# Kernel tuning notes

Hardware: AMD Instinct MI355X
Metric: run time of the kernel (lower is better)

## Reference

```python
import jax, jax.numpy as jnp
import numpy as np

H = 1024      # hidden_size
NH = 16       # num_heads
DH = H // NH  # size_per_head
RV = 32       # relative_vocab_size
B, S = 1, 2048


def setup_inputs() -> dict:
    key = jax.random.key(0)
    ks = jax.random.split(key, 12)
    std = 0.02
    inp = {
        'x': jax.random.normal(ks[0], (B, S, H), jnp.float32),
        'att_mask': jnp.ones((B, S, S), jnp.int32),
        'relative_att_ids': jax.random.randint(ks[1], (B, S, S), 0, RV),
        'Wq': jax.random.normal(ks[2], (H, H), jnp.float32) * std,
        'bq': jnp.zeros((H,), jnp.float32),
        'Wk': jax.random.normal(ks[3], (H, H), jnp.float32) * std,
        'bk': jnp.zeros((H,), jnp.float32),
        'Wv': jax.random.normal(ks[4], (H, H), jnp.float32) * std,
        'bv': jnp.zeros((H,), jnp.float32),
        'rel_emb': jax.random.normal(ks[5], (RV, NH, DH), jnp.float32) * 0.5,
        'rel_bias': jnp.zeros((RV, NH), jnp.float32),
        'Wo': jax.random.normal(ks[6], (H, H), jnp.float32) * std,
        'bo': jnp.zeros((H,), jnp.float32),
    }
    return inp


def reference(x, att_mask, relative_att_ids, Wq, bq, Wk, bk, Wv, bv,
              rel_emb, rel_bias, Wo, bo):
    b, s, _ = x.shape
    # multi-head projections: [b, s, nh, dh]
    q = (x @ Wq + bq).reshape(b, s, NH, DH)
    k = (x @ Wk + bk).reshape(b, s, NH, DH)
    v = (x @ Wv + bv).reshape(b, s, NH, DH)

    # content scores: [b, q, k, h]
    content = jnp.einsum('bqhd,bkhd->bqkh', q, k)

    # relative scores over vocab: [b, q, r, h], then gather per key position
    all_rel = jnp.einsum('bqhd,rhd->bqrh', q, rel_emb) + rel_bias
    rel_scores = jnp.take_along_axis(all_rel, relative_att_ids[..., None], axis=2)

    scores = (content + rel_scores) / jnp.sqrt(jnp.asarray(DH, x.dtype))
    scores = scores + (-10000.0) * (1.0 - att_mask[..., None].astype(scores.dtype))

    probs = jax.nn.softmax(scores, axis=2)  # softmax over key dim (axis=-2)
    ctx = jnp.einsum('bqkh,bkhd->bqhd', probs, v).reshape(b, s, H)
    return ctx @ Wo + bo
```

## Files before the change

### kernel.cpp

```cpp
#include <hip/hip_runtime.h>
#include <hip/hip_bf16.h>

#define S 2048
#define H 1024
#define NH 16
#define DH 64
#define RV 32
#define BK 32
#define NSPLIT 2
#define SKEYS (S / NSPLIT)

typedef __hip_bfloat16 bf16;
typedef short bf16x8 __attribute__((ext_vector_type(8)));
typedef float f32x4 __attribute__((ext_vector_type(4)));

__device__ __forceinline__ float b2f(bf16 v) { return __bfloat162float(v); }
__device__ __forceinline__ unsigned short f2bbits(float x) {
    __hip_bfloat16 b = __float2bfloat16(x);
    return *reinterpret_cast<unsigned short*>(&b);
}
__device__ __forceinline__ float ldf(const void* p, int i, int f) {
    return f ? ((const float*)p)[i] : b2f(((const bf16*)p)[i]);
}
__device__ __forceinline__ void gl_lds16(const bf16* g, bf16* l) {
    __builtin_amdgcn_global_load_lds(
        (const __attribute__((address_space(1))) void*)g,
        (__attribute__((address_space(3))) void*)l,
        16, 0, 0);
}

__global__ void detect_dtype(const unsigned int* __restrict__ xw,
                             int* __restrict__ flag)
{
    __shared__ int cnt;
    if (threadIdx.x == 0) cnt = 0;
    __syncthreads();
    unsigned int w = xw[threadIdx.x];
    unsigned int ex = ((w & 0xffffu) >> 7) & 0xffu;
    int big = (ex > 134u) ? 1 : 0;
    #pragma unroll
    for (int off = 32; off > 0; off >>= 1) big += __shfl_xor(big, off, 64);
    if ((threadIdx.x & 63) == 0) atomicAdd(&cnt, big);
    __syncthreads();
    if (threadIdx.x == 0) *flag = (cnt > 60) ? 1 : 0;
}

__global__ __launch_bounds__(256) void pack_rm(
    const int* __restrict__ rel_ids, const int* __restrict__ att_mask,
    unsigned char* __restrict__ PBg)
{
    int i = blockIdx.x * 256 + threadIdx.x;
    int4 rid = ((const int4*)rel_ids)[i];
    int4 msk = ((const int4*)att_mask)[i];
    uchar4 o;
    o.x = (unsigned char)(rid.x | ((msk.x == 0) << 7));
    o.y = (unsigned char)(rid.y | ((msk.y == 0) << 7));
    o.z = (unsigned char)(rid.z | ((msk.z == 0) << 7));
    o.w = (unsigned char)(rid.w | ((msk.w == 0) << 7));
    ((uchar4*)PBg)[i] = o;
}

__global__ __launch_bounds__(256) void convert_x(
    const void* __restrict__ x, bf16* __restrict__ xb,
    const int* __restrict__ flag)
{
    const int i = (blockIdx.x * 256 + threadIdx.x) * 4;
    if (*flag) {
        float4 v = ((const float4*)x)[i >> 2];
        ushort4 o;
        o.x = f2bbits(v.x); o.y = f2bbits(v.y);
        o.z = f2bbits(v.z); o.w = f2bbits(v.w);
        *(ushort4*)&xb[i] = o;
    } else {
        ((ushort4*)xb)[i >> 2] = ((const ushort4*)x)[i >> 2];
    }
}

__global__ __launch_bounds__(256) void wtrans(
    const void* __restrict__ W0, const void* __restrict__ W1,
    const void* __restrict__ W2, const void* __restrict__ W3,
    bf16* __restrict__ T0, bf16* __restrict__ T1,
    bf16* __restrict__ T2, bf16* __restrict__ T3,
    const int* __restrict__ flag)
{
    const void* W; bf16* T;
    switch (blockIdx.z) {
        case 0:  W = W0; T = T0; break;
        case 1:  W = W1; T = T1; break;
        case 2:  W = W2; T = T2; break;
        default: W = W3; T = T3; break;
    }
    const int f = *flag;
    __shared__ unsigned short Ts[64][68];
    const int t = threadIdx.x;
    const int tx = t & 15, ty = t >> 4;
    const int n0 = blockIdx.x * 64;
    const int k0 = blockIdx.y * 64;
    #pragma unroll
    for (int it = 0; it < 4; ++it) {
        int k = ty + it * 16;
        int base = (k0 + k) * H + n0 + tx * 4;
        #pragma unroll
        for (int e = 0; e < 4; ++e)
            Ts[k][tx * 4 + e] = f2bbits(ldf(W, base + e, f));
    }
    __syncthreads();
    #pragma unroll
    for (int it = 0; it < 4; ++it) {
        int n = ty + it * 16;
        ushort4 o;
        o.x = Ts[tx * 4 + 0][n];
        o.y = Ts[tx * 4 + 1][n];
        o.z = Ts[tx * 4 + 2][n];
        o.w = Ts[tx * 4 + 3][n];
        *(ushort4*)&T[(size_t)(n0 + n) * H + k0 + tx * 4] = o;
    }
}

__global__ __launch_bounds__(256) void vtrans(
    const bf16* __restrict__ Vb, bf16* __restrict__ VT)
{
    __shared__ unsigned short Ts[64][68];
    const int t = threadIdx.x;
    const int tx = t & 15, ty = t >> 4;
    const int s0 = blockIdx.x * 64;
    const int h0 = blockIdx.y * 64;
    #pragma unroll
    for (int it = 0; it < 4; ++it) {
        int s = ty + it * 16;
        *(ushort4*)&Ts[s][tx * 4] =
            *(const ushort4*)&Vb[(size_t)(s0 + s) * H + h0 + tx * 4];
    }
    __syncthreads();
    #pragma unroll
    for (int it = 0; it < 4; ++it) {
        int hh = ty + it * 16;
        ushort4 o;
        o.x = Ts[tx * 4 + 0][hh];
        o.y = Ts[tx * 4 + 1][hh];
        o.z = Ts[tx * 4 + 2][hh];
        o.w = Ts[tx * 4 + 3][hh];
        *(ushort4*)&VT[(size_t)(h0 + hh) * S + s0 + tx * 4] = o;
    }
}

template<int BM, int BN>
__device__ __forceinline__ void gemm_bt_core(
    const bf16* __restrict__ A, const bf16* __restrict__ BT,
    f32x4 (&acc)[BM / 32][BN / 32])
{
    constexpr int MT = BM / 32, NT = BN / 32;
    const int tid = threadIdx.x;
    const int w = tid >> 6, lane = tid & 63;
    const int l15 = lane & 15, quad = lane >> 4;
    const int wm = (w & 1) * (BM / 2), wn = (w >> 1) * (BN / 2);
    const int rowb = blockIdx.y * BM;
    const int colb = blockIdx.x * BN;

    __shared__ bf16 As[BM * BK];
    __shared__ bf16 Bs[BN * BK];

    for (int kb = 0; kb < H; kb += BK) {
        #pragma unroll
        for (int j = 0; j < BM / 64; ++j) {
            int i = j * 256 + w * 64 + lane;
            gl_lds16(&A[(size_t)(rowb + (i >> 2)) * H + kb + (i & 3) * 8],
                     &As[(size_t)(j * 256 + w * 64) * 8]);
        }
        #pragma unroll
        for (int j = 0; j < BN / 64; ++j) {
            int i = j * 256 + w * 64 + lane;
            gl_lds16(&BT[(size_t)(colb + (i >> 2)) * H + kb + (i & 3) * 8],
                     &Bs[(size_t)(j * 256 + w * 64) * 8]);
        }
        __syncthreads();

        bf16x8 af[MT], bfr[NT];
        #pragma unroll
        for (int mt = 0; mt < MT; ++mt)
            af[mt] = *(const bf16x8*)&As[(wm + mt * 16 + l15) * BK + quad * 8];
        #pragma unroll
        for (int nt = 0; nt < NT; ++nt)
            bfr[nt] = *(const bf16x8*)&Bs[(wn + nt * 16 + l15) * BK + quad * 8];
        #pragma unroll
        for (int mt = 0; mt < MT; ++mt)
            #pragma unroll
            for (int nt = 0; nt < NT; ++nt)
                acc[mt][nt] = __builtin_amdgcn_mfma_f32_16x16x32_bf16(
                    af[mt], bfr[nt], acc[mt][nt], 0, 0, 0);
        __syncthreads();
    }
}

__global__ __launch_bounds__(256) void qkv_mfma(
    const bf16* __restrict__ xb,
    const bf16* __restrict__ WTq, const bf16* __restrict__ WTk,
    const bf16* __restrict__ WTv,
    const void* __restrict__ bq, const void* __restrict__ bk,
    const void* __restrict__ bv,
    bf16* __restrict__ Qb, bf16* __restrict__ Kb, bf16* __restrict__ Vb,
    const int* __restrict__ flag)
{
    const bf16* BT; const void* bias; bf16* out; float scale;
    if (blockIdx.z == 0)      { BT = WTq; bias = bq; out = Qb; scale = 1.0f;   }
    else if (blockIdx.z == 1) { BT = WTk; bias = bk; out = Kb; scale = 0.125f; }
    else                      { BT = WTv; bias = bv; out = Vb; scale = 1.0f;   }
    const int f = *flag;

    f32x4 acc[4][2];
    #pragma unroll
    for (int a = 0; a < 4; ++a)
        #pragma unroll
        for (int b = 0; b < 2; ++b) acc[a][b] = (f32x4)0.f;

    gemm_bt_core<128, 64>(xb, BT, acc);

    const int tid = threadIdx.x;
    const int w = tid >> 6, lane = tid & 63;
    const int l15 = lane & 15, quad = lane >> 4;
    const int wm = (w & 1) * 64, wn = (w >> 1) * 32;
    const int rowb = blockIdx.y * 128;
    const int colb = blockIdx.x * 64;

    float bvv[2];
    #pragma unroll
    for (int nt = 0; nt < 2; ++nt)
        bvv[nt] = ldf(bias, colb + wn + nt * 16 + l15, f);

    #pragma unroll
    for (int mt = 0; mt < 4; ++mt)
        #pragma unroll
        for (int nt = 0; nt < 2; ++nt)
            #pragma unroll
            for (int r = 0; r < 4; ++r) {
                int m = rowb + wm + mt * 16 + quad * 4 + r;
                int n = colb + wn + nt * 16 + l15;
                out[(size_t)m * H + n] =
                    __float2bfloat16((acc[mt][nt][r] + bvv[nt]) * scale);
            }
}

__global__ __launch_bounds__(256) void out_mfma(
    const bf16* __restrict__ Cb, const bf16* __restrict__ WoT,
    const void* __restrict__ bias, void* __restrict__ out,
    const int* __restrict__ flag)
{
    const int f = *flag;
    f32x4 acc[2][2];
    #pragma unroll
    for (int a = 0; a < 2; ++a)
        #pragma unroll
        for (int b = 0; b < 2; ++b) acc[a][b] = (f32x4)0.f;

    gemm_bt_core<64, 64>(Cb, WoT, acc);

    const int tid = threadIdx.x;
    const int w = tid >> 6, lane = tid & 63;
    const int l15 = lane & 15, quad = lane >> 4;
    const int wm = (w & 1) * 32, wn = (w >> 1) * 32;
    const int rowb = blockIdx.y * 64;
    const int colb = blockIdx.x * 64;

    float bvv[2];
    #pragma unroll
    for (int nt = 0; nt < 2; ++nt)
        bvv[nt] = ldf(bias, colb + wn + nt * 16 + l15, f);

    #pragma unroll
    for (int mt = 0; mt < 2; ++mt)
        #pragma unroll
        for (int nt = 0; nt < 2; ++nt)
            #pragma unroll
            for (int r = 0; r < 4; ++r) {
                int m = rowb + wm + mt * 16 + quad * 4 + r;
                int n = colb + wn + nt * 16 + l15;
                float v = acc[mt][nt][r] + bvv[nt];
                if (f) ((float*)out)[(size_t)m * H + n] = v;
                else   ((bf16*)out)[(size_t)m * H + n] = __float2bfloat16(v);
            }
}

__global__ __launch_bounds__(256, 4) void attn_mfma(
    const bf16* __restrict__ Qb, const bf16* __restrict__ Kb,
    const bf16* __restrict__ VT,
    const void* __restrict__ rel_emb, const void* __restrict__ rel_bias,
    const unsigned char* __restrict__ PBg,
    float* __restrict__ Op, float* __restrict__ Lp,
    const int* __restrict__ flag)
{
    const int h = blockIdx.x;
    const int qb = blockIdx.y;
    const int split = blockIdx.z;
    const int q0 = qb * 64;
    const int kt0 = split * SKEYS;
    const int tid = threadIdx.x;
    const int w = tid >> 6;
    const int lane = tid & 63;
    const int l15 = lane & 15;
    const int quad = lane >> 4;
    const int f = *flag;

    __shared__ short Ks[64][80];
    __shared__ short Vs[64][80];
    __shared__ float Rl[64][33];
    __shared__ float Rbias[32];
    union SharedU {
        short Es[32][64];
        short Ps[64][72];
    };
    __shared__ SharedU U;

    const unsigned char* pbrow = PBg + (size_t)(q0 + w * 16 + l15) * S;

    uint4 kp[2], vp[2];
    unsigned int pb[4];
    {
        #pragma unroll
        for (int j = 0; j < 2; ++j) {
            int slot = j * 256 + tid;
            int r = slot >> 3, c = slot & 7;
            kp[j] = *(const uint4*)&Kb[(size_t)(kt0 + r) * H + h * DH + c * 8];
            vp[j] = *(const uint4*)&VT[(size_t)(h * DH + r) * S + kt0 + c * 8];
        }
        #pragma unroll
        for (int nt = 0; nt < 4; ++nt)
            pb[nt] = *(const unsigned int*)&pbrow[kt0 + nt * 16 + quad * 4];
    }

    bf16x8 aq0, aq1;
    {
        const bf16* qrow = Qb + (size_t)(q0 + w * 16 + l15) * H + h * DH;
        aq0 = *(const bf16x8*)&qrow[quad * 8];
        aq1 = *(const bf16x8*)&qrow[32 + quad * 8];
    }

    {
        int r = tid >> 3, c8 = (tid & 7) * 8;
        unsigned short os[8];
        if (f) {
            const float* src = (const float*)rel_emb + (r * NH + h) * DH + c8;
            #pragma unroll
            for (int e = 0; e < 8; ++e) os[e] = f2bbits(src[e] * 0.125f);
        } else {
            const bf16* src = (const bf16*)rel_emb + (r * NH + h) * DH + c8;
            #pragma unroll
            for (int e = 0; e < 8; ++e) os[e] = f2bbits(b2f(src[e]) * 0.125f);
        }
        *(ushort4*)&U.Es[r][c8]     = *(ushort4*)&os[0];
        *(ushort4*)&U.Es[r][c8 + 4] = *(ushort4*)&os[4];
        if (tid < RV) Rbias[tid] = ldf(rel_bias, tid * NH + h, f) * 0.125f;
    }
    __syncthreads();

    #pragma unroll
    for (int nt = 0; nt < 2; ++nt) {
        bf16x8 be0 = *(const bf16x8*)&U.Es[nt * 16 + l15][quad * 8];
        bf16x8 be1 = *(const bf16x8*)&U.Es[nt * 16 + l15][32 + quad * 8];
        f32x4 c = (f32x4)0.f;
        c = __builtin_amdgcn_mfma_f32_16x16x32_bf16(aq0, be0, c, 0, 0, 0);
        c = __builtin_amdgcn_mfma_f32_16x16x32_bf16(aq1, be1, c, 0, 0, 0);
        float rb = Rbias[nt * 16 + l15];
        #pragma unroll
        for (int r = 0; r < 4; ++r)
            Rl[w * 16 + quad * 4 + r][nt * 16 + l15] = c[r] + rb;
    }
    __syncthreads();

    f32x4 O[4];
    #pragma unroll
    for (int i = 0; i < 4; ++i) O[i] = (f32x4)0.f;
    float llocal = 0.f;
    const float* rlrow = &Rl[w * 16 + l15][0];

    for (int kt = kt0; kt < kt0 + SKEYS; kt += 64) {
        #pragma unroll
        for (int j = 0; j < 2; ++j) {
            int slot = j * 256 + tid;
            int r = slot >> 3, c = slot & 7;
            *(uint4*)&Ks[r][c * 8] = kp[j];
            *(uint4*)&Vs[r][c * 8] = vp[j];
        }
        unsigned int pbc[4];
        #pragma unroll
        for (int nt = 0; nt < 4; ++nt) pbc[nt] = pb[nt];
        __syncthreads();

        if (kt + 64 < kt0 + SKEYS) {
            #pragma unroll
            for (int j = 0; j < 2; ++j) {
                int slot = j * 256 + tid;
                int r = slot >> 3, c = slot & 7;
                kp[j] = *(const uint4*)&Kb[(size_t)(kt + 64 + r) * H + h * DH + c * 8];
                vp[j] = *(const uint4*)&VT[(size_t)(h * DH + r) * S + kt + 64 + c * 8];
            }
            #pragma unroll
            for (int nt = 0; nt < 4; ++nt)
                pb[nt] = *(const unsigned int*)&pbrow[kt + 64 + nt * 16 + quad * 4];
        }

        f32x4 sc[4];
        #pragma unroll
        for (int nt = 0; nt < 4; ++nt) {
            bf16x8 ak0 = *(const bf16x8*)&Ks[nt * 16 + l15][quad * 8];
            bf16x8 ak1 = *(const bf16x8*)&Ks[nt * 16 + l15][32 + quad * 8];
            f32x4 c = (f32x4)0.f;
            c = __builtin_amdgcn_mfma_f32_16x16x32_bf16(ak0, aq0, c, 0, 0, 0);
            c = __builtin_amdgcn_mfma_f32_16x16x32_bf16(ak1, aq1, c, 0, 0, 0);
            sc[nt] = c;
        }

        #pragma unroll
        for (int nt = 0; nt < 4; ++nt) {
            unsigned int pw = pbc[nt];
            #pragma unroll
            for (int r = 0; r < 4; ++r) {
                unsigned int b = pw >> (8 * r);
                float rl = rlrow[b & 63u];
                float p = __expf(sc[nt][r] + rl);
                p = (b & 0x80u) ? 0.f : p;
                sc[nt][r] = p;
            }
            llocal += (sc[nt][0] + sc[nt][1]) + (sc[nt][2] + sc[nt][3]);
            ushort4 o;
            o.x = f2bbits(sc[nt][0]); o.y = f2bbits(sc[nt][1]);
            o.z = f2bbits(sc[nt][2]); o.w = f2bbits(sc[nt][3]);
            *(ushort4*)&U.Ps[w * 16 + l15][nt * 16 + quad * 4] = o;
        }

        bf16x8 ap0 = *(const bf16x8*)&U.Ps[w * 16 + l15][quad * 8];
        bf16x8 ap1 = *(const bf16x8*)&U.Ps[w * 16 + l15][32 + quad * 8];
        #pragma unroll
        for (int dt = 0; dt < 4; ++dt) {
            bf16x8 bv0 = *(const bf16x8*)&Vs[dt * 16 + l15][quad * 8];
            bf16x8 bv1 = *(const bf16x8*)&Vs[dt * 16 + l15][32 + quad * 8];
            O[dt] = __builtin_amdgcn_mfma_f32_16x16x32_bf16(ap0, bv0, O[dt], 0, 0, 0);
            O[dt] = __builtin_amdgcn_mfma_f32_16x16x32_bf16(ap1, bv1, O[dt], 0, 0, 0);
        }
        __syncthreads();
    }

    float lsum = llocal;
    lsum += __shfl_xor(lsum, 16, 64);
    lsum += __shfl_xor(lsum, 32, 64);

    const size_t base = ((size_t)split * NH + h) * 32 + qb;
    float* Ob = Op + base * 4096;
    #pragma unroll
    for (int r = 0; r < 4; ++r) {
        int qr = w * 16 + quad * 4 + r;
        #pragma unroll
        for (int dt = 0; dt < 4; ++dt)
            Ob[qr * 64 + dt * 16 + l15] = O[dt][r];
    }
    if (quad == 0) Lp[base * 64 + w * 16 + l15] = lsum;
}

__global__ __launch_bounds__(256) void reduce_splits(
    const float* __restrict__ Op, const float* __restrict__ Lp,
    bf16* __restrict__ Cb)
{
    const int h = blockIdx.x;
    const int qb = blockIdx.y;
    const int q0 = qb * 64;
    const int tid = threadIdx.x;
    const int q = tid >> 2;
    const int d0 = (tid & 3) * 16;

    const size_t b0 = ((size_t)0 * NH + h) * 32 + qb;
    const size_t b1 = ((size_t)1 * NH + h) * 32 + qb;

    float l = Lp[b0 * 64 + q] + Lp[b1 * 64 + q];
    float inv = 1.0f / l;

    const float4* O0 = (const float4*)(Op + b0 * 4096 + q * 64 + d0);
    const float4* O1 = (const float4*)(Op + b1 * 4096 + q * 64 + d0);
    bf16* outp = Cb + (size_t)(q0 + q) * H + h * DH + d0;
    #pragma unroll
    for (int j = 0; j < 4; ++j) {
        float4 v0 = O0[j], v1 = O1[j];
        ushort4 o;
        o.x = f2bbits((v0.x + v1.x) * inv);
        o.y = f2bbits((v0.y + v1.y) * inv);
        o.z = f2bbits((v0.z + v1.z) * inv);
        o.w = f2bbits((v0.w + v1.w) * inv);
        *(ushort4*)&outp[j * 4] = o;
    }
}

extern "C" void kernel_launch(void* const* d_in, const int* in_sizes, int n_in,
                              void* d_out, int out_size, void* d_ws, size_t ws_size,
                              hipStream_t stream)
{
    const void* x        = d_in[0];
    const int*  att_mask = (const int*)d_in[1];
    const int*  rel_ids  = (const int*)d_in[2];
    const void* Wq = d_in[3];
    const void* bq = d_in[4];
    const void* Wk = d_in[5];
    const void* bk = d_in[6];
    const void* Wv = d_in[7];
    const void* bv = d_in[8];
    const void* rel_emb  = d_in[9];
    const void* rel_bias = d_in[10];
    const void* Wo = d_in[11];
    const void* bo = d_in[12];

    char* p = (char*)d_ws;
    bf16* xb  = (bf16*)p; p += (size_t)S * H * 2;
    bf16* WTq = (bf16*)p; p += (size_t)H * H * 2;
    bf16* WTk = (bf16*)p; p += (size_t)H * H * 2;
    bf16* WTv = (bf16*)p; p += (size_t)H * H * 2;
    bf16* WoT = (bf16*)p; p += (size_t)H * H * 2;
    bf16* Qb  = (bf16*)p; p += (size_t)S * H * 2;
    bf16* Kb  = (bf16*)p; p += (size_t)S * H * 2;
    bf16* Vb  = (bf16*)p; p += (size_t)S * H * 2;
    bf16* VT  = (bf16*)p; p += (size_t)S * H * 2;
    bf16* Cb  = (bf16*)p; p += (size_t)S * H * 2;
    unsigned char* PBg = (unsigned char*)p; p += (size_t)S * S;
    float* Op = (float*)p; p += (size_t)NSPLIT * NH * 32 * 64 * 64 * 4;
    float* Lp = (float*)p; p += (size_t)NSPLIT * NH * 32 * 64 * 4;
    int* flag = (int*)p;

    detect_dtype<<<1, 256, 0, stream>>>((const unsigned int*)x, flag);

    pack_rm<<<(S * S) / 1024, 256, 0, stream>>>(rel_ids, att_mask, PBg);
    convert_x<<<(S * H) / 1024, 256, 0, stream>>>(x, xb, flag);
    wtrans<<<dim3(H / 64, H / 64, 4), 256, 0, stream>>>(
        Wq, Wk, Wv, Wo, WTq, WTk, WTv, WoT, flag);

    qkv_mfma<<<dim3(H / 64, S / 128, 3), 256, 0, stream>>>(
        xb, WTq, WTk, WTv, bq, bk, bv, Qb, Kb, Vb, flag);

    vtrans<<<dim3(S / 64, H / 64), 256, 0, stream>>>(Vb, VT);

    attn_mfma<<<dim3(NH, S / 64, NSPLIT), 256, 0, stream>>>(
        Qb, Kb, VT, rel_emb, rel_bias, PBg, Op, Lp, flag);

    reduce_splits<<<dim3(NH, S / 64), 256, 0, stream>>>(Op, Lp, Cb);

    out_mfma<<<dim3(H / 64, S / 64), 256, 0, stream>>>(Cb, WoT, bo, d_out, flag);
}
```

Baseline: 260.6 us.

## Load K/V fragments directly from global, drop LDS staging, split keys four ways

Removes the K and V shared-memory tiles and the register prefetch, so each wave loads its MFMA operands straight from global memory (relying on L1/L2 for reuse across the four waves). This eliminates two block barriers per key tile and frees LDS and registers. In exchange, the launch-bounds occupancy hint rises to 6 and the key dimension is split four ways instead of two, with the reduce kernel generalized to sum NSPLIT partials. The risks are redundant global traffic, since each wave rereads the same K/V, less latency hiding with no prefetch, and larger partial buffers for the reduction.

```diff
diff --git a/kernel.cpp b/kernel.cpp
--- a/kernel.cpp
+++ b/kernel.cpp
@@ -7,7 +7,7 @@
 #define DH 64
 #define RV 32
 #define BK 32
-#define NSPLIT 2
+#define NSPLIT 4
 #define SKEYS (S / NSPLIT)
 
 typedef __hip_bfloat16 bf16;
@@ -280,7 +280,7 @@
             }
 }
 
-__global__ __launch_bounds__(256, 4) void attn_mfma(
+__global__ __launch_bounds__(256, 6) void attn_mfma(
     const bf16* __restrict__ Qb, const bf16* __restrict__ Kb,
     const bf16* __restrict__ VT,
     const void* __restrict__ rel_emb, const void* __restrict__ rel_bias,
@@ -300,8 +300,6 @@
     const int quad = lane >> 4;
     const int f = *flag;
 
-    __shared__ short Ks[64][80];
-    __shared__ short Vs[64][80];
     __shared__ float Rl[64][33];
     __shared__ float Rbias[32];
     union SharedU {
@@ -309,23 +307,6 @@
         short Ps[64][72];
     };
     __shared__ SharedU U;
-
-    const unsigned char* pbrow = PBg + (size_t)(q0 + w * 16 + l15) * S;
-
-    uint4 kp[2], vp[2];
-    unsigned int pb[4];
-    {
-        #pragma unroll
-        for (int j = 0; j < 2; ++j) {
-            int slot = j * 256 + tid;
-            int r = slot >> 3, c = slot & 7;
-            kp[j] = *(const uint4*)&Kb[(size_t)(kt0 + r) * H + h * DH + c * 8];
-            vp[j] = *(const uint4*)&VT[(size_t)(h * DH + r) * S + kt0 + c * 8];
-        }
-        #pragma unroll
-        for (int nt = 0; nt < 4; ++nt)
-            pb[nt] = *(const unsigned int*)&pbrow[kt0 + nt * 16 + quad * 4];
-    }
 
     bf16x8 aq0, aq1;
     {
@@ -371,38 +352,20 @@
     for (int i = 0; i < 4; ++i) O[i] = (f32x4)0.f;
     float llocal = 0.f;
     const float* rlrow = &Rl[w * 16 + l15][0];
+    const unsigned char* pbrow = PBg + (size_t)(q0 + w * 16 + l15) * S;
 
     for (int kt = kt0; kt < kt0 + SKEYS; kt += 64) {
-        #pragma unroll
-        for (int j = 0; j < 2; ++j) {
-            int slot = j * 256 + tid;
-            int r = slot >> 3, c = slot & 7;
-            *(uint4*)&Ks[r][c * 8] = kp[j];
-            *(uint4*)&Vs[r][c * 8] = vp[j];
-        }
         unsigned int pbc[4];
         #pragma unroll
-        for (int nt = 0; nt < 4; ++nt) pbc[nt] = pb[nt];
-        __syncthreads();
-
-        if (kt + 64 < kt0 + SKEYS) {
-            #pragma unroll
-            for (int j = 0; j < 2; ++j) {
-                int slot = j * 256 + tid;
-                int r = slot >> 3, c = slot & 7;
-                kp[j] = *(const uint4*)&Kb[(size_t)(kt + 64 + r) * H + h * DH + c * 8];
-                vp[j] = *(const uint4*)&VT[(size_t)(h * DH + r) * S + kt + 64 + c * 8];
-            }
-            #pragma unroll
-            for (int nt = 0; nt < 4; ++nt)
-                pb[nt] = *(const unsigned int*)&pbrow[kt + 64 + nt * 16 + quad * 4];
-        }
+        for (int nt = 0; nt < 4; ++nt)
+            pbc[nt] = *(const unsigned int*)&pbrow[kt + nt * 16 + quad * 4];
 
         f32x4 sc[4];
         #pragma unroll
         for (int nt = 0; nt < 4; ++nt) {
-            bf16x8 ak0 = *(const bf16x8*)&Ks[nt * 16 + l15][quad * 8];
-            bf16x8 ak1 = *(const bf16x8*)&Ks[nt * 16 + l15][32 + quad * 8];
+            const bf16* krow = Kb + (size_t)(kt + nt * 16 + l15) * H + h * DH;
+            bf16x8 ak0 = *(const bf16x8*)&krow[quad * 8];
+            bf16x8 ak1 = *(const bf16x8*)&krow[32 + quad * 8];
             f32x4 c = (f32x4)0.f;
             c = __builtin_amdgcn_mfma_f32_16x16x32_bf16(ak0, aq0, c, 0, 0, 0);
             c = __builtin_amdgcn_mfma_f32_16x16x32_bf16(ak1, aq1, c, 0, 0, 0);
@@ -431,12 +394,12 @@
         bf16x8 ap1 = *(const bf16x8*)&U.Ps[w * 16 + l15][32 + quad * 8];
         #pragma unroll
         for (int dt = 0; dt < 4; ++dt) {
-            bf16x8 bv0 = *(const bf16x8*)&Vs[dt * 16 + l15][quad * 8];
-            bf16x8 bv1 = *(const bf16x8*)&Vs[dt * 16 + l15][32 + quad * 8];
+            const bf16* vrow = VT + (size_t)(h * DH + dt * 16 + l15) * S + kt;
+            bf16x8 bv0 = *(const bf16x8*)&vrow[quad * 8];
+            bf16x8 bv1 = *(const bf16x8*)&vrow[32 + quad * 8];
             O[dt] = __builtin_amdgcn_mfma_f32_16x16x32_bf16(ap0, bv0, O[dt], 0, 0, 0);
             O[dt] = __builtin_amdgcn_mfma_f32_16x16x32_bf16(ap1, bv1, O[dt], 0, 0, 0);
         }
-        __syncthreads();
     }
 
     float lsum = llocal;
@@ -466,23 +429,34 @@
     const int q = tid >> 2;
     const int d0 = (tid & 3) * 16;
 
-    const size_t b0 = ((size_t)0 * NH + h) * 32 + qb;
-    const size_t b1 = ((size_t)1 * NH + h) * 32 + qb;
-
-    float l = Lp[b0 * 64 + q] + Lp[b1 * 64 + q];
+    float l = 0.f;
+    float acc[16];
+    #pragma unroll
+    for (int j = 0; j < 16; ++j) acc[j] = 0.f;
+
+    #pragma unroll
+    for (int s = 0; s < NSPLIT; ++s) {
+        const size_t b = ((size_t)s * NH + h) * 32 + qb;
+        l += Lp[b * 64 + q];
+        const float4* Os = (const float4*)(Op + b * 4096 + q * 64 + d0);
+        #pragma unroll
+        for (int j = 0; j < 4; ++j) {
+            float4 v = Os[j];
+            acc[j * 4 + 0] += v.x;
+            acc[j * 4 + 1] += v.y;
+            acc[j * 4 + 2] += v.z;
+            acc[j * 4 + 3] += v.w;
+        }
+    }
     float inv = 1.0f / l;
-
-    const float4* O0 = (const float4*)(Op + b0 * 4096 + q * 64 + d0);
-    const float4* O1 = (const float4*)(Op + b1 * 4096 + q * 64 + d0);
     bf16* outp = Cb + (size_t)(q0 + q) * H + h * DH + d0;
     #pragma unroll
     for (int j = 0; j < 4; ++j) {
-        float4 v0 = O0[j], v1 = O1[j];
         ushort4 o;
-        o.x = f2bbits((v0.x + v1.x) * inv);
-        o.y = f2bbits((v0.y + v1.y) * inv);
-        o.z = f2bbits((v0.z + v1.z) * inv);
-        o.w = f2bbits((v0.w + v1.w) * inv);
+        o.x = f2bbits(acc[j * 4 + 0] * inv);
+        o.y = f2bbits(acc[j * 4 + 1] * inv);
+        o.z = f2bbits(acc[j * 4 + 2] * inv);
+        o.w = f2bbits(acc[j * 4 + 3] * inv);
         *(ushort4*)&outp[j * 4] = o;
     }
 }
```

After: 344.8 us. 1.32x slower.
